# Optimization experiments

Hardware: AMD Instinct MI355X
Metric: run time of the kernel (lower is better)

## Reference

```python
import jax, jax.numpy as jnp
import numpy as np

B, T, D = 8, 16, 1024
N, K, H = 16, 8, 128   # q heads, kv heads, head dim
S = 8192               # cache size
CUR = 4096             # tokens already in cache
ROPE_THETA = 1000000
EPS = 1e-6
LARGE_NEGATIVE = jnp.finfo(jnp.bfloat16).min


def setup_inputs() -> dict:
    key = jax.random.key(0)
    ks = jax.random.split(key, 8)
    w = 0.02  # realistic weight scale
    return {
        "x": jax.random.normal(ks[0], (B, T, D), jnp.float32),
        "Wq": jax.random.normal(ks[1], (D, N, H), jnp.float32) * w,
        "Wk": jax.random.normal(ks[2], (D, K, H), jnp.float32) * w,
        "Wv": jax.random.normal(ks[3], (D, K, H), jnp.float32) * w,
        "Wo": jax.random.normal(ks[4], (N, H, D), jnp.float32) * w,
        "q_scale": jnp.ones((H,), jnp.float32),
        "k_scale": jnp.ones((H,), jnp.float32),
        "k_cache": jax.random.normal(ks[5], (B, S, K, H), jnp.float32),
        "v_cache": jax.random.normal(ks[6], (B, S, K, H), jnp.float32),
        "segment_ids": jnp.ones((B, T), jnp.int32),
        "start_ind": jnp.zeros((B,), jnp.int32),  # already resolved (= left_pads)
        "cur_ind": CUR,
    }


def _rmsnorm(x, scale, eps=EPS):
    xf = x.astype(jnp.float32)
    y = xf * jax.lax.rsqrt(jnp.mean(xf * xf, axis=-1, keepdims=True) + eps)
    return (y * scale).astype(x.dtype)


def _rope_sincos(positions, head_dim):
    frac = jnp.arange(0, head_dim, 2, dtype=jnp.float32) / head_dim
    inv_freq = 1.0 / (ROPE_THETA ** frac)
    ang = jnp.einsum("BT,k->BTk", positions.astype(jnp.float32), inv_freq,
                     precision=jax.lax.Precision.HIGHEST)
    return jnp.sin(ang), jnp.cos(ang)


def _apply_rope(x, sin, cos):
    x1, x2 = x[..., : x.shape[-1] // 2], x[..., x.shape[-1] // 2 :]
    sin, cos = sin[:, :, None, :], cos[:, :, None, :]
    return jnp.concatenate([x1 * cos - x2 * sin, x2 * cos + x1 * sin], axis=-1).astype(x.dtype)


def reference(x, Wq, Wk, Wv, Wo, q_scale, k_scale, k_cache, v_cache,
              segment_ids, start_ind, cur_ind):
    b, t, _ = x.shape
    n_rep = N // K
    scale = H ** -0.5

    # projections + per-head RMSNorm on q/k
    q = _rmsnorm(jnp.einsum("BTD,DNH->BTNH", x, Wq), q_scale)
    k = _rmsnorm(jnp.einsum("BSD,DKH->BSKH", x, Wk), k_scale)
    v = jnp.einsum("BSD,DKH->BSKH", x, Wv)

    # start index: resolved from left pads on first call
    left_pads = jnp.sum(jnp.cumsum(segment_ids != 0, axis=-1) == 0, -1).astype(jnp.int32)
    start = jnp.where(start_ind < 0, left_pads, start_ind)

    # positions from segment ids, offset by cache cursor
    rel = jax.vmap(lambda row: jnp.where(row != 0, jnp.arange(t) - jnp.argmax(row), 2 ** 30))(segment_ids)
    pos = rel + cur_ind
    sin, cos = _rope_sincos(pos, H)
    q = _apply_rope(q, sin, cos)
    k = _apply_rope(k, sin, cos)

    # KV cache append
    kc = jax.lax.dynamic_update_slice(k_cache, k, (0, cur_ind, 0, 0))
    vc = jax.lax.dynamic_update_slice(v_cache, v, (0, cur_ind, 0, 0))

    # GQA attention against full cache
    qg = q.reshape((b, t, K, n_rep, H))
    logits = jnp.einsum("BTKGH,BSKH->BTSKG", qg, kc) * scale

    q_pos = cur_ind + jnp.arange(t, dtype=jnp.int32)[None, :] - start[:, None]
    ts = jnp.arange(S, dtype=jnp.int32)
    kv_seg = (ts[None, :] >= start[:, None]) & (ts[None, :] < cur_ind + t)
    k_pos = ts[None, :] - start[:, None]
    causal = k_pos[:, None, :] <= q_pos[:, :, None]
    seg_mask = kv_seg[:, None, :] == segment_ids[:, :, None]
    mask = (causal & seg_mask)[:, :, :, None, None]

    logits = jnp.where(mask, logits, LARGE_NEGATIVE)
    w = jax.nn.softmax(logits.astype(jnp.float32), axis=2).astype(logits.dtype)
    o = jnp.einsum("BTSKG,BSKH->BTKGH", w, vc).reshape((b, t, N, H))
    return jnp.einsum("BTNH,NHD->BTD", o, Wo)
```

## Files before the change

### kernel.cpp

```cpp
#include <hip/hip_runtime.h>

#define BB 8
#define TT 16
#define DD 1024
#define NN 16
#define KHN 8
#define HH 128
#define SS 8192
#define NPART 8

typedef __attribute__((ext_vector_type(8))) short bf16x8;
typedef __attribute__((ext_vector_type(4))) float f32x4;

__device__ __forceinline__ unsigned short f2bf(float f) {
  unsigned u = __builtin_bit_cast(unsigned, f);
  u += 0x7FFFu + ((u >> 16) & 1u);
  return (unsigned short)(u >> 16);
}
__device__ __forceinline__ float bf2f(unsigned short h) {
  unsigned u = ((unsigned)h) << 16;
  return __builtin_bit_cast(float, u);
}
__device__ __forceinline__ f32x4 mfma16(bf16x8 a, bf16x8 b, f32x4 c) {
  return __builtin_amdgcn_mfma_f32_16x16x32_bf16(a, b, c, 0, 0, 0);
}
__device__ __forceinline__ void pack4(unsigned short* dst, float a, float b, float c, float d) {
  unsigned lo = (unsigned)f2bf(a) | ((unsigned)f2bf(b) << 16);
  unsigned hi = (unsigned)f2bf(c) | ((unsigned)f2bf(d) << 16);
  *(uint2*)dst = make_uint2(lo, hi);
}

__global__ __launch_bounds__(256) void k_wtrans(
    const float* __restrict__ Wq, const float* __restrict__ Wk,
    const float* __restrict__ Wv, const float* __restrict__ Wo,
    unsigned short* __restrict__ Wt1, unsigned short* __restrict__ Wt2) {
  __shared__ __align__(16) unsigned short Tl[64][66];
  const int tid = threadIdx.x;
  const int z = blockIdx.z;
  const float* src; int K, N; unsigned short* dst;
  if (z == 0)      { src = Wq; K = 1024; N = 2048; dst = Wt1; }
  else if (z == 1) { src = Wk; K = 1024; N = 1024; dst = Wt1 + (size_t)2048 * 1024; }
  else if (z == 2) { src = Wv; K = 1024; N = 1024; dst = Wt1 + (size_t)3072 * 1024; }
  else             { src = Wo; K = 2048; N = 1024; dst = Wt2; }
  const int n0 = blockIdx.x * 64, k0 = blockIdx.y * 64;
  if (n0 >= N || k0 >= K) return;
  {
    const int r = tid >> 4, c4 = (tid & 15) << 2;
#pragma unroll
    for (int p = 0; p < 4; ++p) {
      const int k = p * 16 + r;
      float4 f = *(const float4*)(src + (size_t)(k0 + k) * N + n0 + c4);
      pack4(&Tl[k][c4], f.x, f.y, f.z, f.w);
    }
  }
  __syncthreads();
  {
    const int c8 = tid & 7, nb = tid >> 3;
#pragma unroll
    for (int p = 0; p < 2; ++p) {
      const int n = p * 32 + nb;
      unsigned short tmp[8];
#pragma unroll
      for (int j = 0; j < 8; ++j) tmp[j] = Tl[c8 * 8 + j][n];
      unsigned short* dp = dst + (size_t)(n0 + n) * K + k0 + c8 * 8;
      *(uint4*)dp = *(const uint4*)&tmp[0];
    }
  }
}

__global__ __launch_bounds__(256) void k_qkv_gemm(
    const float* __restrict__ x, const unsigned short* __restrict__ Wt1,
    float* __restrict__ qkv) {
  const int tid = threadIdx.x, lane = tid & 63, wv = tid >> 6;
  const int cc = lane & 15, g = lane >> 4;
  const int m0 = blockIdx.x * 32, n0 = blockIdx.y * 128;
  const int rt = wv >> 1, cb0 = (wv & 1) * 64;
  const int m = m0 + rt * 16 + cc;
  f32x4 acc[4];
#pragma unroll
  for (int i = 0; i < 4; ++i) acc[i] = (f32x4)0.0f;

#pragma unroll 4
  for (int k0 = 0; k0 < 1024; k0 += 32) {
    float4 fa = *(const float4*)(x + (size_t)m * 1024 + k0 + g * 8);
    float4 fb = *(const float4*)(x + (size_t)m * 1024 + k0 + g * 8 + 4);
    bf16x8 af;
    af[0] = (short)f2bf(fa.x); af[1] = (short)f2bf(fa.y);
    af[2] = (short)f2bf(fa.z); af[3] = (short)f2bf(fa.w);
    af[4] = (short)f2bf(fb.x); af[5] = (short)f2bf(fb.y);
    af[6] = (short)f2bf(fb.z); af[7] = (short)f2bf(fb.w);
#pragma unroll
    for (int ct = 0; ct < 4; ++ct) {
      const int n = n0 + cb0 + ct * 16 + cc;
      bf16x8 bf = *(const bf16x8*)(Wt1 + (size_t)n * 1024 + k0 + g * 8);
      acc[ct] = mfma16(af, bf, acc[ct]);
    }
  }
#pragma unroll
  for (int ct = 0; ct < 4; ++ct)
#pragma unroll
    for (int r = 0; r < 4; ++r) {
      int row = m0 + rt * 16 + g * 4 + r;
      int col = n0 + cb0 + ct * 16 + cc;
      qkv[(size_t)row * 4096 + col] = acc[ct][r];
    }
}

__global__ __launch_bounds__(128) void k_normrope(
    const float* __restrict__ qkv, const float* __restrict__ qs,
    const float* __restrict__ ks, const int* __restrict__ seg,
    const int* __restrict__ cur_p,
    unsigned short* __restrict__ qa, unsigned short* __restrict__ ka,
    unsigned short* __restrict__ va) {
  __shared__ float lv[128];
  __shared__ float red[2];
  const int row = blockIdx.x, b = row >> 4, t = row & 15;
  const int hid = blockIdx.y;
  const int h = threadIdx.x;
  float val;
  if (hid < 16)      val = qkv[row * 4096 + hid * 128 + h];
  else if (hid < 24) val = qkv[row * 4096 + 2048 + (hid - 16) * 128 + h];
  else               val = qkv[row * 4096 + 3072 + (hid - 24) * 128 + h];

  if (hid >= 24) {
    int kh = hid - 24;
    va[((b * KHN + kh) * TT + t) * 128 + h] = f2bf(val);
    return;
  }
  float ss = val * val;
#pragma unroll
  for (int m = 1; m < 64; m <<= 1) ss += __shfl_xor(ss, m, 64);
  int wid = threadIdx.x >> 6, lane = threadIdx.x & 63;
  if (lane == 0) red[wid] = ss;
  __syncthreads();
  float mean = (red[0] + red[1]) * (1.0f / 128.0f);
  float scl = (hid < 16) ? qs[h] : ks[h];
  float nrm = val * (1.0f / sqrtf(mean + 1e-6f)) * scl;
  lv[h] = nrm;
  __syncthreads();
  float prt = lv[h ^ 64];
  const int cur = cur_p[0];
  int first = TT;
#pragma unroll
  for (int i = TT - 1; i >= 0; --i)
    if (seg[b * TT + i] != 0) first = i;
  float posf;
  if (seg[b * TT + t] != 0) posf = (float)(t - first + cur);
  else                      posf = (float)(1073741824 + cur);
  int j = h & 63;
  float inv = powf(1.0e6f, -((float)j) * (1.0f / 64.0f));
  float ang = posf * inv;
  float sn = sinf(ang), cs = cosf(ang);
  float outv = (h < 64) ? (nrm * cs - prt * sn) : (nrm * cs + prt * sn);
  if (hid < 16) {
    int kh = hid >> 1, gq = hid & 1;
    qa[((b * KHN + kh) * 32 + gq * 16 + t) * 128 + h] =
        f2bf(outv * 0.08838834764831845f);
  } else {
    int kh = hid - 16;
    ka[((b * KHN + kh) * TT + t) * 128 + h] = f2bf(outv);
  }
}

__global__ __launch_bounds__(256, 2) void k_attn(
    const float* __restrict__ kcache, const float* __restrict__ vcache,
    const unsigned short* __restrict__ qa, const unsigned short* __restrict__ ka,
    const unsigned short* __restrict__ va, const int* __restrict__ seg,
    const int* __restrict__ sind, const int* __restrict__ cur_p,
    float* __restrict__ partO, float* __restrict__ partML) {
  __shared__ __align__(16) unsigned short Kl[4][32][132];
  __shared__ __align__(16) unsigned short Pl[4][32][40];
  __shared__ float mls[2][32][2];
  const int tid = threadIdx.x, wv = tid >> 6, lane = tid & 63;
  const int cc = lane & 15, g = lane >> 4;
  const int pair = blockIdx.x, b = pair >> 3, kh = pair & 7;
  const int qi = blockIdx.y;
  const int cur = cur_p[0];
  const int len = cur + TT;
  int start_b = sind[b];
  if (start_b < 0) {
    int first = TT;
#pragma unroll
    for (int i = TT - 1; i >= 0; --i)
      if (seg[b * TT + i] != 0) first = i;
    start_b = first;
  }
  const int NTt = (len + 31) >> 5;
  const int L = (NTt + NPART - 1) / NPART;
  const int tlo = qi * L;
  const int thi = (tlo + L < NTt) ? (tlo + L) : NTt;

  bf16x8 qf[2][4];
  {
    const unsigned short* qb = qa + ((size_t)pair * 32) * 128;
#pragma unroll
    for (int rb = 0; rb < 2; ++rb)
#pragma unroll
      for (int kk = 0; kk < 4; ++kk)
        qf[rb][kk] = *(const bf16x8*)(qb + (rb * 16 + cc) * 128 + kk * 32 + g * 8);
  }
  const float* kcb = kcache + (size_t)b * (SS * 1024) + kh * 128;
  const float* vcb = vcache + (size_t)b * (SS * 1024) + kh * 128;
  const unsigned short* knb = ka + (size_t)(b * KHN + kh) * (TT * 128);
  const unsigned short* vnb = va + (size_t)(b * KHN + kh) * (TT * 128);

  f32x4 acc[2][8];
  float mreg[2][4], lreg[2][4];
#pragma unroll
  for (int rb = 0; rb < 2; ++rb) {
#pragma unroll
    for (int hb = 0; hb < 8; ++hb) acc[rb][hb] = (f32x4)0.0f;
#pragma unroll
    for (int r = 0; r < 4; ++r) { mreg[rb][r] = -1e30f; lreg[rb][r] = 0.0f; }
  }

  for (int tile = tlo + wv; tile < thi; tile += 4) {
    const int ts0 = tile << 5;
    if (ts0 + 32 <= cur) {
#pragma unroll
      for (int i = 0; i < 16; ++i) {
        int ch = lane + (i << 6);
        int r = ch >> 5, c4 = (ch & 31) << 2;
        float4 f = *(const float4*)(kcb + (size_t)(ts0 + r) * 1024 + c4);
        pack4(&Kl[wv][r][c4], f.x, f.y, f.z, f.w);
      }
    } else {
#pragma unroll
      for (int i = 0; i < 16; ++i) {
        int ch = lane + (i << 6);
        int r = ch >> 5, c4 = (ch & 31) << 2;
        int ts = ts0 + r;
        if (ts < cur) {
          float4 f = *(const float4*)(kcb + (size_t)ts * 1024 + c4);
          pack4(&Kl[wv][r][c4], f.x, f.y, f.z, f.w);
        } else {
          int tr = ts - cur; if (tr > TT - 1) tr = TT - 1;
          ushort4 u = *(const ushort4*)(knb + tr * 128 + c4);
          *(ushort4*)&Kl[wv][r][c4] = u;
        }
      }
    }
    __builtin_amdgcn_wave_barrier();
    bf16x8 vf[8];
    if (ts0 + 32 <= cur) {
#pragma unroll
      for (int hb = 0; hb < 8; ++hb) {
        int hc = hb * 16 + cc;
#pragma unroll
        for (int j = 0; j < 8; ++j) {
          int ts = ts0 + g * 8 + j;
          vf[hb][j] = (short)f2bf(vcb[(size_t)ts * 1024 + hc]);
        }
      }
    } else {
#pragma unroll
      for (int hb = 0; hb < 8; ++hb) {
        int hc = hb * 16 + cc;
#pragma unroll
        for (int j = 0; j < 8; ++j) {
          int ts = ts0 + g * 8 + j;
          float vvf;
          if (ts < cur) vvf = vcb[(size_t)ts * 1024 + hc];
          else { int tr = ts - cur; if (tr > TT - 1) tr = TT - 1; vvf = bf2f(vnb[tr * 128 + hc]); }
          vf[hb][j] = (short)f2bf(vvf);
        }
      }
    }
    f32x4 s[2][2];
#pragma unroll
    for (int rb = 0; rb < 2; ++rb)
#pragma unroll
      for (int cb = 0; cb < 2; ++cb) s[rb][cb] = (f32x4)0.0f;
#pragma unroll
    for (int kk = 0; kk < 4; ++kk) {
#pragma unroll
      for (int cb = 0; cb < 2; ++cb) {
        const unsigned short* kp = &Kl[wv][cb * 16 + cc][kk * 32 + g * 8];
        uint2 lo = *(const uint2*)kp;
        uint2 hi = *(const uint2*)(kp + 4);
        bf16x8 kf = __builtin_bit_cast(bf16x8, make_uint4(lo.x, lo.y, hi.x, hi.y));
        s[0][cb] = mfma16(qf[0][kk], kf, s[0][cb]);
        s[1][cb] = mfma16(qf[1][kk], kf, s[1][cb]);
      }
    }
    float al[2][4];
#pragma unroll
    for (int rb = 0; rb < 2; ++rb) {
#pragma unroll
      for (int r = 0; r < 4; ++r) {
        const int tq = g * 4 + r;
#pragma unroll
        for (int cb = 0; cb < 2; ++cb) {
          int ts = ts0 + cb * 16 + cc;
          bool ok = (ts >= start_b) && (ts <= cur + tq);
          if (!ok) s[rb][cb][r] = -1e30f;
        }
        float tm = fmaxf(s[rb][0][r], s[rb][1][r]);
#pragma unroll
        for (int m = 1; m < 16; m <<= 1) tm = fmaxf(tm, __shfl_xor(tm, m, 64));
        float mn = fmaxf(mreg[rb][r], tm);
        float a = __expf(mreg[rb][r] - mn);
        float p0 = (s[rb][0][r] < -1e29f) ? 0.0f : __expf(s[rb][0][r] - mn);
        float p1 = (s[rb][1][r] < -1e29f) ? 0.0f : __expf(s[rb][1][r] - mn);
        s[rb][0][r] = p0; s[rb][1][r] = p1;
        float rs = p0 + p1;
#pragma unroll
        for (int m = 1; m < 16; m <<= 1) rs += __shfl_xor(rs, m, 64);
        lreg[rb][r] = lreg[rb][r] * a + rs;
        mreg[rb][r] = mn;
        al[rb][r] = a;
      }
    }
#pragma unroll
    for (int rb = 0; rb < 2; ++rb)
#pragma unroll
      for (int cb = 0; cb < 2; ++cb)
#pragma unroll
        for (int r = 0; r < 4; ++r)
          Pl[wv][rb * 16 + g * 4 + r][cb * 16 + cc] = f2bf(s[rb][cb][r]);
    __builtin_amdgcn_wave_barrier();
    bf16x8 pf[2];
#pragma unroll
    for (int rb = 0; rb < 2; ++rb)
      pf[rb] = *(const bf16x8*)&Pl[wv][rb * 16 + cc][g * 8];
#pragma unroll
    for (int rb = 0; rb < 2; ++rb)
#pragma unroll
      for (int hb = 0; hb < 8; ++hb) {
        f32x4 t = acc[rb][hb];
#pragma unroll
        for (int r = 0; r < 4; ++r) t[r] *= al[rb][r];
        acc[rb][hb] = mfma16(pf[rb], vf[hb], t);
      }
  }

  float* Oscr = (float*)&Kl[0][0][0];
  auto dump = [&](int sid) {
#pragma unroll
    for (int rb = 0; rb < 2; ++rb)
#pragma unroll
      for (int hb = 0; hb < 8; ++hb)
#pragma unroll
        for (int r = 0; r < 4; ++r)
          Oscr[(sid * 32 + rb * 16 + g * 4 + r) * 128 + hb * 16 + cc] = acc[rb][hb][r];
    if (cc == 0) {
#pragma unroll
      for (int rb = 0; rb < 2; ++rb)
#pragma unroll
        for (int r = 0; r < 4; ++r) {
          mls[sid][rb * 16 + g * 4 + r][0] = mreg[rb][r];
          mls[sid][rb * 16 + g * 4 + r][1] = lreg[rb][r];
        }
    }
  };
  auto mergefrom = [&](int sid) {
    float a0s[2][4], a1s[2][4];
#pragma unroll
    for (int rb = 0; rb < 2; ++rb)
#pragma unroll
      for (int r = 0; r < 4; ++r) {
        int row = rb * 16 + g * 4 + r;
        float mp = mls[sid][row][0], lp = mls[sid][row][1];
        float M = fmaxf(mreg[rb][r], mp);
        float a0 = __expf(mreg[rb][r] - M), a1 = __expf(mp - M);
        lreg[rb][r] = lreg[rb][r] * a0 + lp * a1;
        mreg[rb][r] = M;
        a0s[rb][r] = a0; a1s[rb][r] = a1;
      }
#pragma unroll
    for (int rb = 0; rb < 2; ++rb)
#pragma unroll
      for (int hb = 0; hb < 8; ++hb)
#pragma unroll
        for (int r = 0; r < 4; ++r) {
          int row = rb * 16 + g * 4 + r;
          acc[rb][hb][r] = acc[rb][hb][r] * a0s[rb][r] +
                           Oscr[(sid * 32 + row) * 128 + hb * 16 + cc] * a1s[rb][r];
        }
  };
  __syncthreads();
  if (wv >= 2) dump(wv - 2);
  __syncthreads();
  if (wv < 2) mergefrom(wv);
  __syncthreads();
  if (wv == 1) dump(0);
  __syncthreads();
  if (wv == 0) {
    mergefrom(0);
    size_t pidx = (size_t)pair * NPART + qi;
#pragma unroll
    for (int rb = 0; rb < 2; ++rb)
#pragma unroll
      for (int hb = 0; hb < 8; ++hb)
#pragma unroll
        for (int r = 0; r < 4; ++r)
          partO[(pidx * 32 + rb * 16 + g * 4 + r) * 128 + hb * 16 + cc] = acc[rb][hb][r];
    if (cc == 0) {
#pragma unroll
      for (int rb = 0; rb < 2; ++rb)
#pragma unroll
        for (int r = 0; r < 4; ++r) {
          partML[pidx * 64 + (rb * 16 + g * 4 + r) * 2 + 0] = mreg[rb][r];
          partML[pidx * 64 + (rb * 16 + g * 4 + r) * 2 + 1] = lreg[rb][r];
        }
    }
  }
}

__global__ __launch_bounds__(256) void k_combine(
    const float* __restrict__ partO, const float* __restrict__ partML,
    unsigned short* __restrict__ obf) {
  __shared__ float sc[NPART][32];
  const int pair = blockIdx.x, b = pair >> 3, kh = pair & 7;
  const int isub = blockIdx.y;
  const int tid = threadIdx.x;
  if (tid < 32) {
    float mm[NPART], ll[NPART];
    float M = -3.0e38f;
#pragma unroll
    for (int p = 0; p < NPART; ++p) {
      mm[p] = partML[((size_t)pair * NPART + p) * 64 + tid * 2 + 0];
      ll[p] = partML[((size_t)pair * NPART + p) * 64 + tid * 2 + 1];
      M = fmaxf(M, mm[p]);
    }
    float denom = 0.0f;
#pragma unroll
    for (int p = 0; p < NPART; ++p) denom += __expf(mm[p] - M) * ll[p];
    float inv = (denom > 0.0f) ? 1.0f / denom : 0.0f;
#pragma unroll
    for (int p = 0; p < NPART; ++p) sc[p][tid] = __expf(mm[p] - M) * inv;
  }
  __syncthreads();
#pragma unroll
  for (int i = 0; i < 4; ++i) {
    int idx = tid + ((isub * 4 + i) << 8);
    int row = idx >> 7, hc = idx & 127;
    float o = 0.0f;
#pragma unroll
    for (int p = 0; p < NPART; ++p)
      o += partO[(((size_t)pair * NPART + p) * 32 + row) * 128 + hc] * sc[p][row];
    int gq = row >> 4, t = row & 15, n = kh * 2 + gq;
    obf[((b * TT + t) * NN + n) * 128 + hc] = f2bf(o);
  }
}

__global__ __launch_bounds__(256) void k_out_gemm(
    const unsigned short* __restrict__ obf, const unsigned short* __restrict__ Wt2,
    float* __restrict__ out) {
  const int tid = threadIdx.x, lane = tid & 63, wv = tid >> 6;
  const int cc = lane & 15, g = lane >> 4;
  const int m0 = blockIdx.x * 32, n0 = blockIdx.y * 64;
  const int rt = wv >> 1, cb0 = (wv & 1) * 32;
  const int m = m0 + rt * 16 + cc;
  f32x4 acc[2];
#pragma unroll
  for (int i = 0; i < 2; ++i) acc[i] = (f32x4)0.0f;

#pragma unroll 4
  for (int k0 = 0; k0 < 2048; k0 += 32) {
    bf16x8 af = *(const bf16x8*)(obf + (size_t)m * 2048 + k0 + g * 8);
#pragma unroll
    for (int ct = 0; ct < 2; ++ct) {
      const int d = n0 + cb0 + ct * 16 + cc;
      bf16x8 bf = *(const bf16x8*)(Wt2 + (size_t)d * 2048 + k0 + g * 8);
      acc[ct] = mfma16(af, bf, acc[ct]);
    }
  }
#pragma unroll
  for (int ct = 0; ct < 2; ++ct)
#pragma unroll
    for (int r = 0; r < 4; ++r)
      out[(size_t)(m0 + rt * 16 + g * 4 + r) * 1024 + n0 + cb0 + ct * 16 + cc] = acc[ct][r];
}

extern "C" void kernel_launch(void* const* d_in, const int* in_sizes, int n_in,
                              void* d_out, int out_size, void* d_ws, size_t ws_size,
                              hipStream_t stream) {
  (void)in_sizes; (void)n_in; (void)out_size; (void)ws_size;
  const float* x   = (const float*)d_in[0];
  const float* Wq  = (const float*)d_in[1];
  const float* Wk  = (const float*)d_in[2];
  const float* Wv  = (const float*)d_in[3];
  const float* Wo  = (const float*)d_in[4];
  const float* qs  = (const float*)d_in[5];
  const float* ks  = (const float*)d_in[6];
  const float* kc  = (const float*)d_in[7];
  const float* vc  = (const float*)d_in[8];
  const int* seg   = (const int*)d_in[9];
  const int* sind  = (const int*)d_in[10];
  const int* curp  = (const int*)d_in[11];
  float* out = (float*)d_out;

  char* ws = (char*)d_ws;
  float*          qkv    = (float*)(ws + 0);
  unsigned short* qa     = (unsigned short*)(ws + 2097152);
  unsigned short* ka     = (unsigned short*)(ws + 2621440);
  unsigned short* va     = (unsigned short*)(ws + 2883584);
  float*          partO  = (float*)(ws + 3145728);
  float*          partML = (float*)(ws + 11534336);
  unsigned short* obf    = (unsigned short*)(ws + 11665408);
  unsigned short* Wt1    = (unsigned short*)(ws + 12189696);
  unsigned short* Wt2    = (unsigned short*)(ws + 20578304);

  k_wtrans<<<dim3(32, 32, 4), 256, 0, stream>>>(Wq, Wk, Wv, Wo, Wt1, Wt2);
  k_qkv_gemm<<<dim3(4, 32), 256, 0, stream>>>(x, Wt1, qkv);
  k_normrope<<<dim3(128, 32), 128, 0, stream>>>(qkv, qs, ks, seg, curp, qa, ka, va);
  k_attn<<<dim3(64, NPART), 256, 0, stream>>>(kc, vc, qa, ka, va, seg, sind, curp, partO, partML);
  k_combine<<<dim3(64, 4), 256, 0, stream>>>(partO, partML, obf);
  k_out_gemm<<<dim3(4, 16), 256, 0, stream>>>(obf, Wt2, out);
}
```

Measured before the change: 139.4 us.

## Software-pipeline K-cache loads into registers one tile ahead

Splits the K tile load into an issue phase (global loads into a register array) and a write phase (pack to LDS). The next tile's K loads are issued mid-iteration, after QK MFMAs and V loads, so they overlap with softmax and PV compute, using two ping-pong register buffers. This aims to hide global memory latency for the fp32 K cache. The cost is a large increase in VGPR pressure (two 16-element float4 arrays), which may lower occupancy or cause spills.

```diff
diff --git a/kernel.cpp b/kernel.cpp
--- a/kernel.cpp
+++ b/kernel.cpp
@@ -214,33 +214,61 @@
     for (int r = 0; r < 4; ++r) { mreg[rb][r] = -1e30f; lreg[rb][r] = 0.0f; }
   }
 
-  for (int tile = tlo + wv; tile < thi; tile += 4) {
+  auto issueK = [&](int tile, float4 (&kr)[16]) {
     const int ts0 = tile << 5;
-    if (ts0 + 32 <= cur) {
-#pragma unroll
-      for (int i = 0; i < 16; ++i) {
-        int ch = lane + (i << 6);
-        int r = ch >> 5, c4 = (ch & 31) << 2;
-        float4 f = *(const float4*)(kcb + (size_t)(ts0 + r) * 1024 + c4);
-        pack4(&Kl[wv][r][c4], f.x, f.y, f.z, f.w);
-      }
-    } else {
-#pragma unroll
-      for (int i = 0; i < 16; ++i) {
-        int ch = lane + (i << 6);
-        int r = ch >> 5, c4 = (ch & 31) << 2;
-        int ts = ts0 + r;
-        if (ts < cur) {
-          float4 f = *(const float4*)(kcb + (size_t)ts * 1024 + c4);
-          pack4(&Kl[wv][r][c4], f.x, f.y, f.z, f.w);
-        } else {
-          int tr = ts - cur; if (tr > TT - 1) tr = TT - 1;
-          ushort4 u = *(const ushort4*)(knb + tr * 128 + c4);
-          *(ushort4*)&Kl[wv][r][c4] = u;
-        }
+#pragma unroll
+    for (int i = 0; i < 16; ++i) {
+      const int ch = lane + (i << 6);
+      const int r = ch >> 5, c4 = (ch & 31) << 2;
+      const int ts = ts0 + r;
+      if (ts < cur) {
+        kr[i] = *(const float4*)(kcb + (size_t)ts * 1024 + c4);
+      } else {
+        int tr = ts - cur; if (tr > TT - 1) tr = TT - 1;
+        uint2 w = *(const uint2*)(knb + tr * 128 + c4);
+        kr[i].x = __builtin_bit_cast(float, w.x);
+        kr[i].y = __builtin_bit_cast(float, w.y);
+      }
+    }
+  };
+  auto writeK = [&](int tile, float4 (&kr)[16]) {
+    const int ts0 = tile << 5;
+#pragma unroll
+    for (int i = 0; i < 16; ++i) {
+      const int ch = lane + (i << 6);
+      const int r = ch >> 5, c4 = (ch & 31) << 2;
+      const int ts = ts0 + r;
+      if (ts < cur) {
+        pack4(&Kl[wv][r][c4], kr[i].x, kr[i].y, kr[i].z, kr[i].w);
+      } else {
+        *(uint2*)&Kl[wv][r][c4] =
+            make_uint2(__builtin_bit_cast(unsigned, kr[i].x),
+                       __builtin_bit_cast(unsigned, kr[i].y));
       }
     }
     __builtin_amdgcn_wave_barrier();
+  };
+
+  auto doTile = [&](int tile, float4 (&kr)[16], int ptile, float4 (&pkr)[16]) {
+    const int ts0 = tile << 5;
+    writeK(tile, kr);
+    f32x4 s[2][2];
+#pragma unroll
+    for (int rb = 0; rb < 2; ++rb)
+#pragma unroll
+      for (int cb = 0; cb < 2; ++cb) s[rb][cb] = (f32x4)0.0f;
+#pragma unroll
+    for (int kk = 0; kk < 4; ++kk) {
+#pragma unroll
+      for (int cb = 0; cb < 2; ++cb) {
+        const unsigned short* kp = &Kl[wv][cb * 16 + cc][kk * 32 + g * 8];
+        uint2 lo = *(const uint2*)kp;
+        uint2 hi = *(const uint2*)(kp + 4);
+        bf16x8 kf = __builtin_bit_cast(bf16x8, make_uint4(lo.x, lo.y, hi.x, hi.y));
+        s[0][cb] = mfma16(qf[0][kk], kf, s[0][cb]);
+        s[1][cb] = mfma16(qf[1][kk], kf, s[1][cb]);
+      }
+    }
     bf16x8 vf[8];
     if (ts0 + 32 <= cur) {
 #pragma unroll
@@ -266,22 +294,9 @@
         }
       }
     }
-    f32x4 s[2][2];
-#pragma unroll
-    for (int rb = 0; rb < 2; ++rb)
-#pragma unroll
-      for (int cb = 0; cb < 2; ++cb) s[rb][cb] = (f32x4)0.0f;
-#pragma unroll
-    for (int kk = 0; kk < 4; ++kk) {
-#pragma unroll
-      for (int cb = 0; cb < 2; ++cb) {
-        const unsigned short* kp = &Kl[wv][cb * 16 + cc][kk * 32 + g * 8];
-        uint2 lo = *(const uint2*)kp;
-        uint2 hi = *(const uint2*)(kp + 4);
-        bf16x8 kf = __builtin_bit_cast(bf16x8, make_uint4(lo.x, lo.y, hi.x, hi.y));
-        s[0][cb] = mfma16(qf[0][kk], kf, s[0][cb]);
-        s[1][cb] = mfma16(qf[1][kk], kf, s[1][cb]);
-      }
+    if (ptile < thi) {
+      issueK(ptile, pkr);
+      __builtin_amdgcn_sched_barrier(0);
     }
     float al[2][4];
 #pragma unroll
@@ -332,6 +347,16 @@
         for (int r = 0; r < 4; ++r) t[r] *= al[rb][r];
         acc[rb][hb] = mfma16(pf[rb], vf[hb], t);
       }
+  };
+
+  {
+    float4 kra[16], krb[16];
+    const int t0 = tlo + wv;
+    if (t0 < thi) issueK(t0, kra);
+    for (int tile = t0; tile < thi; tile += 8) {
+      doTile(tile, kra, tile + 4, krb);
+      if (tile + 4 < thi) doTile(tile + 4, krb, tile + 8, kra);
+    }
   }
 
   float* Oscr = (float*)&Kl[0][0][0];
```

Result: slower. 283.1 us (+103.1%).

## Stage V tiles through LDS with coalesced loads and double split-K partitions

Applied to the files above, without the earlier changes.

V tiles are now loaded with coalesced float4 reads, converted to bf16 and staged in the per-wave LDS buffer that K uses, reusing it after the QK MFMAs. The MFMA V fragments are then read back from LDS instead of being fetched with strided scalar global loads. The number of sequence partitions is also doubled to 16, which gives more parallel blocks and requires larger partial-output workspace offsets. The trade-off is extra LDS traffic, more wave barriers, and more partial results for the combine kernel to reduce.

```diff
diff --git a/kernel.cpp b/kernel.cpp
--- a/kernel.cpp
+++ b/kernel.cpp
@@ -7,7 +7,7 @@
 #define KHN 8
 #define HH 128
 #define SS 8192
-#define NPART 8
+#define NPART 16
 
 typedef __attribute__((ext_vector_type(8))) short bf16x8;
 typedef __attribute__((ext_vector_type(4))) float f32x4;
@@ -216,6 +216,7 @@
 
   for (int tile = tlo + wv; tile < thi; tile += 4) {
     const int ts0 = tile << 5;
+    __builtin_amdgcn_wave_barrier();
     if (ts0 + 32 <= cur) {
 #pragma unroll
       for (int i = 0; i < 16; ++i) {
@@ -241,31 +242,6 @@
       }
     }
     __builtin_amdgcn_wave_barrier();
-    bf16x8 vf[8];
-    if (ts0 + 32 <= cur) {
-#pragma unroll
-      for (int hb = 0; hb < 8; ++hb) {
-        int hc = hb * 16 + cc;
-#pragma unroll
-        for (int j = 0; j < 8; ++j) {
-          int ts = ts0 + g * 8 + j;
-          vf[hb][j] = (short)f2bf(vcb[(size_t)ts * 1024 + hc]);
-        }
-      }
-    } else {
-#pragma unroll
-      for (int hb = 0; hb < 8; ++hb) {
-        int hc = hb * 16 + cc;
-#pragma unroll
-        for (int j = 0; j < 8; ++j) {
-          int ts = ts0 + g * 8 + j;
-          float vvf;
-          if (ts < cur) vvf = vcb[(size_t)ts * 1024 + hc];
-          else { int tr = ts - cur; if (tr > TT - 1) tr = TT - 1; vvf = bf2f(vnb[tr * 128 + hc]); }
-          vf[hb][j] = (short)f2bf(vvf);
-        }
-      }
-    }
     f32x4 s[2][2];
 #pragma unroll
     for (int rb = 0; rb < 2; ++rb)
@@ -283,6 +259,32 @@
         s[1][cb] = mfma16(qf[1][kk], kf, s[1][cb]);
       }
     }
+    __builtin_amdgcn_wave_barrier();
+    if (ts0 + 32 <= cur) {
+#pragma unroll
+      for (int i = 0; i < 16; ++i) {
+        int ch = lane + (i << 6);
+        int r = ch >> 5, c4 = (ch & 31) << 2;
+        float4 f = *(const float4*)(vcb + (size_t)(ts0 + r) * 1024 + c4);
+        pack4(&Kl[wv][r][c4], f.x, f.y, f.z, f.w);
+      }
+    } else {
+#pragma unroll
+      for (int i = 0; i < 16; ++i) {
+        int ch = lane + (i << 6);
+        int r = ch >> 5, c4 = (ch & 31) << 2;
+        int ts = ts0 + r;
+        if (ts < cur) {
+          float4 f = *(const float4*)(vcb + (size_t)ts * 1024 + c4);
+          pack4(&Kl[wv][r][c4], f.x, f.y, f.z, f.w);
+        } else {
+          int tr = ts - cur; if (tr > TT - 1) tr = TT - 1;
+          ushort4 u = *(const ushort4*)(vnb + tr * 128 + c4);
+          *(ushort4*)&Kl[wv][r][c4] = u;
+        }
+      }
+    }
+    __builtin_amdgcn_wave_barrier();
     float al[2][4];
 #pragma unroll
     for (int rb = 0; rb < 2; ++rb) {
@@ -323,6 +325,14 @@
 #pragma unroll
     for (int rb = 0; rb < 2; ++rb)
       pf[rb] = *(const bf16x8*)&Pl[wv][rb * 16 + cc][g * 8];
+    bf16x8 vf[8];
+#pragma unroll
+    for (int hb = 0; hb < 8; ++hb) {
+      int hc = hb * 16 + cc;
+#pragma unroll
+      for (int j = 0; j < 8; ++j)
+        vf[hb][j] = (short)Kl[wv][g * 8 + j][hc];
+    }
 #pragma unroll
     for (int rb = 0; rb < 2; ++rb)
 #pragma unroll
@@ -497,10 +507,10 @@
   unsigned short* ka     = (unsigned short*)(ws + 2621440);
   unsigned short* va     = (unsigned short*)(ws + 2883584);
   float*          partO  = (float*)(ws + 3145728);
-  float*          partML = (float*)(ws + 11534336);
-  unsigned short* obf    = (unsigned short*)(ws + 11665408);
-  unsigned short* Wt1    = (unsigned short*)(ws + 12189696);
-  unsigned short* Wt2    = (unsigned short*)(ws + 20578304);
+  float*          partML = (float*)(ws + 19922944);
+  unsigned short* obf    = (unsigned short*)(ws + 20185088);
+  unsigned short* Wt1    = (unsigned short*)(ws + 20709376);
+  unsigned short* Wt2    = (unsigned short*)(ws + 29097984);
 
   k_wtrans<<<dim3(32, 32, 4), 256, 0, stream>>>(Wq, Wk, Wv, Wo, Wt1, Wt2);
   k_qkv_gemm<<<dim3(4, 32), 256, 0, stream>>>(x, Wt1, qkv);
```

Result: slower. 153.9 us (+10.4%).
